# Optimization experiments

Hardware: AMD Instinct MI355X
Metric: run time of the kernel (lower is better)

Reference implementation:

```python
import jax, jax.numpy as jnp
import numpy as np

B, N, C = 8, 1374, 768
H = 12
HD = C // H  # 64
HIDDEN = int(C * 4.0)  # 3072
EPS = 1e-5


def setup_inputs() -> dict:
    key = jax.random.key(0)
    ks = jax.random.split(key, 12)
    s = 0.02
    return {
        "x": jax.random.normal(ks[0], (B, N, C), jnp.float32),
        "rope_freqs": jax.random.normal(ks[1], (1, N, 1, HD), jnp.float32),
        "ln1_g": jnp.ones((C,), jnp.float32),
        "ln1_b": jnp.zeros((C,), jnp.float32),
        "qkv_w": jax.random.normal(ks[2], (3 * C, C), jnp.float32) * s,
        "qkv_b": jnp.zeros((3 * C,), jnp.float32),
        "proj_w": jax.random.normal(ks[3], (C, C), jnp.float32) * s,
        "proj_b": jnp.zeros((C,), jnp.float32),
        "ln2_g": jnp.ones((C,), jnp.float32),
        "ln2_b": jnp.zeros((C,), jnp.float32),
        "w1": jax.random.normal(ks[4], (HIDDEN, C), jnp.float32) * s,
        "b1": jnp.zeros((HIDDEN,), jnp.float32),
        "w2": jax.random.normal(ks[5], (HIDDEN, C), jnp.float32) * s,
        "b2": jnp.zeros((HIDDEN,), jnp.float32),
        "w3": jax.random.normal(ks[6], (C, HIDDEN), jnp.float32) * s,
        "b3": jnp.zeros((C,), jnp.float32),
    }


def _layernorm(x, g, b):
    mu = jnp.mean(x, axis=-1, keepdims=True)
    var = jnp.mean(jnp.square(x - mu), axis=-1, keepdims=True)
    return (x - mu) * jax.lax.rsqrt(var + EPS) * g + b


def _rotate_half(x):
    x1, x2 = jnp.split(x, 2, axis=-1)
    return jnp.concatenate([-x2, x1], axis=-1)


def _apply_rope(q, k, freqs):
    # freqs: [1, N, 1, HD] -> [1, 1, N, HD] (matches torch permute(0,2,1,3))
    f = jnp.transpose(freqs, (0, 2, 1, 3))
    cos, sin = jnp.cos(f), jnp.sin(f)
    q_rot = q * cos + _rotate_half(q) * sin
    k_rot = k * cos + _rotate_half(k) * sin
    return q_rot, k_rot


def reference(x, rope_freqs, ln1_g, ln1_b, qkv_w, qkv_b, proj_w, proj_b,
              ln2_g, ln2_b, w1, b1, w2, b2, w3, b3):
    scale = HD ** -0.5
    # --- Attention branch ---
    h = _layernorm(x, ln1_g, ln1_b)
    qkv = jnp.einsum('bnc,dc->bnd', h, qkv_w) + qkv_b          # [B,N,3C]
    qkv = qkv.reshape(B, N, 3, H, HD).transpose(2, 0, 3, 1, 4)  # [3,B,H,N,HD]
    q, k, v = qkv[0], qkv[1], qkv[2]
    # rope_freqs covers all N tokens -> n_special = 0 path
    q, k = _apply_rope(q, k, rope_freqs)
    attn = jnp.einsum('bhnd,bhmd->bhnm', q, k) * scale          # [B,H,N,N]
    attn = jax.nn.softmax(attn, axis=-1)
    o = jnp.einsum('bhnm,bhmd->bhnd', attn, v)                  # [B,H,N,HD]
    o = o.transpose(0, 2, 1, 3).reshape(B, N, C)
    o = jnp.einsum('bnc,dc->bnd', o, proj_w) + proj_b
    x = x + o
    # --- SwiGLU MLP branch ---
    h2 = _layernorm(x, ln2_g, ln2_b)
    x1 = jnp.einsum('bnc,hc->bnh', h2, w1) + b1
    x2 = jnp.einsum('bnc,hc->bnh', h2, w2) + b2
    hid = jax.nn.silu(x1) * x2
    mlp_out = jnp.einsum('bnh,ch->bnc', hid, w3) + b3
    return x + mlp_out
```

## Files before the change

### kernel.cpp

```cpp
#include <hip/hip_runtime.h>
#include <stdint.h>

#define B_ 8
#define N_ 1374
#define C_ 768
#define H_ 12
#define HD_ 64
#define HID_ 3072
#define M_ (B_*N_)
#define MPAD_ 11008
#define QT_ 22
#define QT2_ 11

typedef __attribute__((ext_vector_type(8))) short short8;
typedef __attribute__((ext_vector_type(4))) float f32x4;
typedef __attribute__((ext_vector_type(4))) _Float16 half4;

__device__ __forceinline__ unsigned short f2bf(float f) {
  unsigned u = __float_as_uint(f);
  u += 0x7FFF + ((u >> 16) & 1);
  return (unsigned short)(u >> 16);
}
__device__ __forceinline__ float bf2f(unsigned short h) {
  return __uint_as_float(((unsigned)h) << 16);
}

#if __has_builtin(__builtin_amdgcn_global_load_lds)
#define HAVE_GLL 1
#endif

__device__ __forceinline__ void gld16(const unsigned short* g, unsigned short* l) {
#ifdef HAVE_GLL
  __builtin_amdgcn_global_load_lds((const __attribute__((address_space(1))) void*)g,
                                   (__attribute__((address_space(3))) void*)l, 16, 0, 0);
#else
  *(short8*)l = *(const short8*)g;
#endif
}

__global__ __launch_bounds__(256) void cvt_kernel(const float* __restrict__ in,
                                                  unsigned short* __restrict__ out, int n4) {
  int id = blockIdx.x * 256 + threadIdx.x;
  if (id >= n4) return;
  float4 v = ((const float4*)in)[id];
  ushort4 o;
  o.x = f2bf(v.x); o.y = f2bf(v.y); o.z = f2bf(v.z); o.w = f2bf(v.w);
  ((ushort4*)out)[id] = o;
}

__global__ __launch_bounds__(256) void ln_kernel(const float* __restrict__ in,
    const float* __restrict__ g, const float* __restrict__ bta,
    unsigned short* __restrict__ out) {
  int row = blockIdx.x;
  int t = threadIdx.x;
  const float* xr = in + (size_t)row * C_;
  float v0 = xr[t], v1 = xr[t + 256], v2 = xr[t + 512];
  float s1 = v0 + v1 + v2;
  float s2 = v0*v0 + v1*v1 + v2*v2;
  for (int off = 1; off < 64; off <<= 1) {
    s1 += __shfl_xor(s1, off, 64);
    s2 += __shfl_xor(s2, off, 64);
  }
  __shared__ float r1[4], r2[4];
  int wave = t >> 6, lane = t & 63;
  if (lane == 0) { r1[wave] = s1; r2[wave] = s2; }
  __syncthreads();
  float tot1 = r1[0] + r1[1] + r1[2] + r1[3];
  float tot2 = r2[0] + r2[1] + r2[2] + r2[3];
  float mu = tot1 * (1.0f / C_);
  float var = tot2 * (1.0f / C_) - mu * mu;
  float rs = rsqrtf(var + 1e-5f);
  size_t ob = (size_t)row * C_;
  out[ob + t]       = f2bf((v0 - mu) * rs * g[t]       + bta[t]);
  out[ob + t + 256] = f2bf((v1 - mu) * rs * g[t + 256] + bta[t + 256]);
  out[ob + t + 512] = f2bf((v2 - mu) * rs * g[t + 512] + bta[t + 512]);
}

template<int EPI>
__global__ __launch_bounds__(256, 2) void gemm_bt(
    const unsigned short* __restrict__ A,
    const unsigned short* __restrict__ W,
    void* __restrict__ outp,
    const float* __restrict__ bias0,
    const float* __restrict__ resid,
    int K, int ldo, int Mvalid)
{
  __shared__ __align__(16) unsigned short As[4096];
  __shared__ __align__(16) unsigned short Bs[4096];
  const int t = threadIdx.x;
  const int lane = t & 63;
  const int wave = t >> 6;
  const int wm = (wave >> 1) * 64;
  const int wn = (wave & 1) * 64;
  const int lr = lane & 15;
  const int lk = (lane >> 4) * 8;
  const int tm0 = blockIdx.y * 128;
  const int tn0 = blockIdx.x * 128;
  const int r0 = t >> 2;
  const int c0 = (t & 3) * 8;
  const unsigned short* ga0 = A + (size_t)(tm0 + r0) * K + c0;
  const unsigned short* ga1 = A + (size_t)(tm0 + 64 + r0) * K + c0;
  const unsigned short* gb0 = W + (size_t)(tn0 + r0) * K + c0;
  const unsigned short* gb1 = W + (size_t)(tn0 + 64 + r0) * K + c0;
  f32x4 zero = {0.f, 0.f, 0.f, 0.f};
  f32x4 acc[4][4];
#pragma unroll
  for (int mi = 0; mi < 4; ++mi)
#pragma unroll
    for (int ni = 0; ni < 4; ++ni) acc[mi][ni] = zero;

  for (int kt = 0; kt < K; kt += 32) {
    __syncthreads();
    gld16(ga0 + kt, &As[t * 8]);
    gld16(ga1 + kt, &As[2048 + t * 8]);
    gld16(gb0 + kt, &Bs[t * 8]);
    gld16(gb1 + kt, &Bs[2048 + t * 8]);
    __syncthreads();
    short8 af[4], bfr[4];
#pragma unroll
    for (int mi = 0; mi < 4; ++mi) af[mi] = *(const short8*)&As[(wm + mi * 16 + lr) * 32 + lk];
#pragma unroll
    for (int ni = 0; ni < 4; ++ni) bfr[ni] = *(const short8*)&Bs[(wn + ni * 16 + lr) * 32 + lk];
#pragma unroll
    for (int mi = 0; mi < 4; ++mi)
#pragma unroll
      for (int ni = 0; ni < 4; ++ni)
        acc[mi][ni] = __builtin_amdgcn_mfma_f32_16x16x32_bf16(af[mi], bfr[ni], acc[mi][ni], 0, 0, 0);
  }
#pragma unroll
  for (int mi = 0; mi < 4; ++mi) {
#pragma unroll
    for (int ni = 0; ni < 4; ++ni) {
      int col = tn0 + wn + ni * 16 + lr;
      float bval = bias0[col];
#pragma unroll
      for (int r = 0; r < 4; ++r) {
        int row = tm0 + wm + mi * 16 + (lane >> 4) * 4 + r;
        float v = acc[mi][ni][r] + bval;
        size_t idx = (size_t)row * ldo + col;
        if (EPI == 0) {
          ((unsigned short*)outp)[idx] = f2bf(v);
        } else if (EPI == 1) {
          if (row < Mvalid) ((float*)outp)[idx] = resid[idx] + v;
        } else {
          if (row < Mvalid) ((float*)outp)[idx] = ((float*)outp)[idx] + v;
        }
      }
    }
  }
}

__global__ __launch_bounds__(256, 2) void gemm_w12_swiglu(
    const unsigned short* __restrict__ A,
    const unsigned short* __restrict__ W1,
    const unsigned short* __restrict__ W2,
    unsigned short* __restrict__ hid,
    const float* __restrict__ b1,
    const float* __restrict__ b2)
{
  __shared__ __align__(16) unsigned short As[4096];
  __shared__ __align__(16) unsigned short B1s[2048];
  __shared__ __align__(16) unsigned short B2s[2048];
  const int t = threadIdx.x;
  const int lane = t & 63;
  const int wave = t >> 6;
  const int wm = (wave >> 1) * 64;
  const int wn = (wave & 1) * 32;
  const int lr = lane & 15;
  const int lg = lane >> 4;
  const int lk = lg * 8;
  const int tm0 = blockIdx.y * 128;
  const int tn0 = blockIdx.x * 64;
  const int r0 = t >> 2;
  const int c0 = (t & 3) * 8;
  const unsigned short* ga0 = A + (size_t)(tm0 + r0) * 768 + c0;
  const unsigned short* ga1 = A + (size_t)(tm0 + 64 + r0) * 768 + c0;
  const unsigned short* g1 = W1 + (size_t)(tn0 + r0) * 768 + c0;
  const unsigned short* g2 = W2 + (size_t)(tn0 + r0) * 768 + c0;
  f32x4 zero = {0.f, 0.f, 0.f, 0.f};
  f32x4 acc1[4][2], acc2[4][2];
#pragma unroll
  for (int mi = 0; mi < 4; ++mi)
#pragma unroll
    for (int ni = 0; ni < 2; ++ni) { acc1[mi][ni] = zero; acc2[mi][ni] = zero; }

  for (int kt = 0; kt < 768; kt += 32) {
    __syncthreads();
    gld16(ga0 + kt, &As[t * 8]);
    gld16(ga1 + kt, &As[2048 + t * 8]);
    gld16(g1 + kt, &B1s[t * 8]);
    gld16(g2 + kt, &B2s[t * 8]);
    __syncthreads();
    short8 af[4], b1f[2], b2f[2];
#pragma unroll
    for (int mi = 0; mi < 4; ++mi) af[mi] = *(const short8*)&As[(wm + mi * 16 + lr) * 32 + lk];
#pragma unroll
    for (int ni = 0; ni < 2; ++ni) {
      b1f[ni] = *(const short8*)&B1s[(wn + ni * 16 + lr) * 32 + lk];
      b2f[ni] = *(const short8*)&B2s[(wn + ni * 16 + lr) * 32 + lk];
    }
#pragma unroll
    for (int mi = 0; mi < 4; ++mi)
#pragma unroll
      for (int ni = 0; ni < 2; ++ni) {
        acc1[mi][ni] = __builtin_amdgcn_mfma_f32_16x16x32_bf16(af[mi], b1f[ni], acc1[mi][ni], 0, 0, 0);
        acc2[mi][ni] = __builtin_amdgcn_mfma_f32_16x16x32_bf16(af[mi], b2f[ni], acc2[mi][ni], 0, 0, 0);
      }
  }
#pragma unroll
  for (int mi = 0; mi < 4; ++mi) {
#pragma unroll
    for (int ni = 0; ni < 2; ++ni) {
      int col = tn0 + wn + ni * 16 + lr;
      float bv1 = b1[col], bv2 = b2[col];
#pragma unroll
      for (int r = 0; r < 4; ++r) {
        int row = tm0 + wm + mi * 16 + lg * 4 + r;
        float a1 = acc1[mi][ni][r] + bv1;
        float a2 = acc2[mi][ni][r] + bv2;
        float h = a1 / (1.f + __expf(-a1)) * a2;
        hid[(size_t)row * HID_ + col] = f2bf(h);
      }
    }
  }
}

__global__ __launch_bounds__(256) void rope_kernel(unsigned short* __restrict__ qkv,
                                                   const float* __restrict__ freqs) {
  int id = blockIdx.x * 256 + threadIdx.x;
  int e = id & 31;
  int hm = id >> 5;
  int head = hm % H_;
  int m = hm / H_;
  int n = m % N_;
  float f1 = freqs[n * HD_ + e];
  float f2 = freqs[n * HD_ + e + 32];
  float c1 = cosf(f1), s1 = sinf(f1);
  float c2 = cosf(f2), s2 = sinf(f2);
  unsigned short* base = qkv + (size_t)m * 2304 + head * HD_ + e;
#pragma unroll
  for (int part = 0; part < 2; ++part) {
    unsigned short* p = base + part * 768;
    float x1 = bf2f(p[0]);
    float x2 = bf2f(p[32]);
    p[0]  = f2bf(x1 * c1 - x2 * s1);
    p[32] = f2bf(x2 * c2 + x1 * s2);
  }
}

__global__ __launch_bounds__(256, 2) void attn_kernel(
    const unsigned short* __restrict__ qkv,
    unsigned short* __restrict__ o2)
{
  __shared__ __align__(16) unsigned short Ks[64 * 80];
  __shared__ __align__(16) _Float16 Vt[64 * 72];
  int bidx = blockIdx.x;
  int qt = bidx % QT2_;
  int bh = bidx / QT2_;
  int head = bh % H_;
  int b = bh / H_;
  int t = threadIdx.x, lane = t & 63, wave = t >> 6;
  int lr = lane & 15, lg = lane >> 4;

  short8 bq[2][2];
#pragma unroll
  for (int s = 0; s < 2; ++s) {
    int m = qt * 128 + wave * 32 + s * 16 + lr;
    int mc = (m < N_) ? m : (N_ - 1);
    const unsigned short* qrow = qkv + (size_t)(b * N_ + mc) * 2304 + head * HD_;
    bq[s][0] = *(const short8*)(qrow + lg * 8);
    bq[s][1] = *(const short8*)(qrow + 32 + lg * 8);
  }

  f32x4 zero = {0.f, 0.f, 0.f, 0.f};
  f32x4 acc[2][4];
#pragma unroll
  for (int s = 0; s < 2; ++s)
#pragma unroll
    for (int dt = 0; dt < 4; ++dt) acc[s][dt] = zero;
  float den[2] = {0.f, 0.f};

  const int vp = t & 31;
  const int vc = t >> 5;

  for (int jt = 0; jt < QT_; ++jt) {
    __syncthreads();
#pragma unroll
    for (int u = t; u < 512; u += 256) {
      int row = u >> 3, c = u & 7;
      int j = jt * 64 + row;
      int jc = (j < N_) ? j : (N_ - 1);
      const unsigned short* src = qkv + (size_t)(b * N_ + jc) * 2304 + 768 + head * HD_ + c * 8;
      *(short8*)&Ks[row * 80 + c * 8] = *(const short8*)src;
    }
    {
      int j0 = jt * 64 + 2 * vp;
      int j1 = j0 + 1;
      int j0c = (j0 < N_) ? j0 : (N_ - 1);
      int j1c = (j1 < N_) ? j1 : (N_ - 1);
      const unsigned short* s0 = qkv + (size_t)(b * N_ + j0c) * 2304 + 1536 + head * HD_ + vc * 8;
      const unsigned short* s1 = qkv + (size_t)(b * N_ + j1c) * 2304 + 1536 + head * HD_ + vc * 8;
      short8 v0 = *(const short8*)s0;
      short8 v1 = *(const short8*)s1;
#pragma unroll
      for (int i = 0; i < 8; ++i) {
        _Float16 lo = (_Float16)bf2f((unsigned short)v0[i]);
        _Float16 hi = (_Float16)bf2f((unsigned short)v1[i]);
        unsigned w = (unsigned)__builtin_bit_cast(unsigned short, lo)
                   | ((unsigned)__builtin_bit_cast(unsigned short, hi) << 16);
        *(unsigned*)&Vt[(vc * 8 + i) * 72 + 2 * vp] = w;
      }
    }
    __syncthreads();
#pragma unroll
    for (int st = 0; st < 4; ++st) {
      short8 ak0 = *(const short8*)&Ks[(st * 16 + lr) * 80 + lg * 8];
      short8 ak1 = *(const short8*)&Ks[(st * 16 + lr) * 80 + 32 + lg * 8];
      int jb = jt * 64 + st * 16 + lg * 4;
      half4 pf[2];
#pragma unroll
      for (int s = 0; s < 2; ++s) {
        f32x4 sc = zero;
        sc = __builtin_amdgcn_mfma_f32_16x16x32_bf16(ak0, bq[s][0], sc, 0, 0, 0);
        sc = __builtin_amdgcn_mfma_f32_16x16x32_bf16(ak1, bq[s][1], sc, 0, 0, 0);
        float dsum = 0.f;
#pragma unroll
        for (int r = 0; r < 4; ++r) {
          float pv = (jb + r < N_) ? __expf(sc[r] * 0.125f) : 0.f;
          dsum += pv;
          pf[s][r] = (_Float16)pv;
        }
        den[s] += dsum;
      }
#pragma unroll
      for (int dt = 0; dt < 4; ++dt) {
        half4 bv = *(const half4*)&Vt[(dt * 16 + lr) * 72 + st * 16 + lg * 4];
        acc[0][dt] = __builtin_amdgcn_mfma_f32_16x16x16f16(pf[0], bv, acc[0][dt], 0, 0, 0);
        acc[1][dt] = __builtin_amdgcn_mfma_f32_16x16x16f16(pf[1], bv, acc[1][dt], 0, 0, 0);
      }
    }
  }
#pragma unroll
  for (int s = 0; s < 2; ++s) {
    den[s] += __shfl_xor(den[s], 16, 64);
    den[s] += __shfl_xor(den[s], 32, 64);
  }
#pragma unroll
  for (int s = 0; s < 2; ++s) {
#pragma unroll
    for (int r = 0; r < 4; ++r) {
      float dm = __shfl(den[s], lg * 4 + r, 64);
      int m = qt * 128 + wave * 32 + s * 16 + lg * 4 + r;
      if (m < N_) {
        float invd = 1.f / dm;
        unsigned short* orow = o2 + (size_t)(b * N_ + m) * C_ + head * HD_;
#pragma unroll
        for (int dt = 0; dt < 4; ++dt)
          orow[dt * 16 + lr] = f2bf(acc[s][dt][r] * invd);
      }
    }
  }
}

extern "C" void kernel_launch(void* const* d_in, const int* in_sizes, int n_in,
                              void* d_out, int out_size, void* d_ws, size_t ws_size,
                              hipStream_t stream) {
  const float* x      = (const float*)d_in[0];
  const float* freqs  = (const float*)d_in[1];
  const float* ln1_g  = (const float*)d_in[2];
  const float* ln1_b  = (const float*)d_in[3];
  const float* qkv_w  = (const float*)d_in[4];
  const float* qkv_b  = (const float*)d_in[5];
  const float* proj_w = (const float*)d_in[6];
  const float* proj_b = (const float*)d_in[7];
  const float* ln2_g  = (const float*)d_in[8];
  const float* ln2_b  = (const float*)d_in[9];
  const float* w1     = (const float*)d_in[10];
  const float* b1     = (const float*)d_in[11];
  const float* w2     = (const float*)d_in[12];
  const float* b2     = (const float*)d_in[13];
  const float* w3     = (const float*)d_in[14];
  const float* b3     = (const float*)d_in[15];
  float* out = (float*)d_out;
  char* ws = (char*)d_ws;

  unsigned short* hB     = (unsigned short*)(ws + 0);
  unsigned short* wqkvB  = (unsigned short*)(ws + 16908288);
  unsigned short* wprojB = (unsigned short*)(ws + 20447232);
  unsigned short* w12B   = (unsigned short*)(ws + 21626880);
  unsigned short* w3B    = (unsigned short*)(ws + 31064064);
  unsigned short* qkvB   = (unsigned short*)(ws + 35782656);
  unsigned short* o2B    = (unsigned short*)(ws + 86507520);
  unsigned short* hidB   = qkvB;

  cvt_kernel<<<1728, 256, 0, stream>>>(qkv_w, wqkvB, 2304 * 768 / 4);
  cvt_kernel<<<576,  256, 0, stream>>>(proj_w, wprojB, 768 * 768 / 4);
  cvt_kernel<<<2304, 256, 0, stream>>>(w1, w12B, 3072 * 768 / 4);
  cvt_kernel<<<2304, 256, 0, stream>>>(w2, w12B + 3072 * 768, 3072 * 768 / 4);
  cvt_kernel<<<2304, 256, 0, stream>>>(w3, w3B, 768 * 3072 / 4);

  ln_kernel<<<M_, 256, 0, stream>>>(x, ln1_g, ln1_b, hB);
  gemm_bt<0><<<dim3(18, 86), 256, 0, stream>>>(hB, wqkvB, qkvB, qkv_b, nullptr, 768, 2304, M_);
  rope_kernel<<<16488, 256, 0, stream>>>(qkvB, freqs);
  attn_kernel<<<B_ * H_ * QT2_, 256, 0, stream>>>(qkvB, o2B);
  gemm_bt<1><<<dim3(6, 86), 256, 0, stream>>>(o2B, wprojB, out, proj_b, x, 768, 768, M_);

  ln_kernel<<<M_, 256, 0, stream>>>(out, ln2_g, ln2_b, hB);
  gemm_w12_swiglu<<<dim3(48, 86), 256, 0, stream>>>(hB, w12B, w12B + 3072 * 768, hidB, b1, b2);
  gemm_bt<3><<<dim3(6, 86), 256, 0, stream>>>(hidB, w3B, out, b3, nullptr, 3072, 768, M_);
}
```

Baseline: 627.5 us.

## Fuse RoPE into QKV GEMM epilogue, merge weight casts, widen GEMM K-step

Removes the standalone rope kernel by applying rotary embedding in the QKV GEMM epilogue, pairing accumulator columns d and d+32 within each wave's 64-column head slice. The five weight-conversion launches become one kernel that dispatches on index range. Both GEMM main loops now load two 32-wide K slices per barrier pair, halving the synchronisation count at the cost of doubled LDS per block, which may reduce occupancy. The fused epilogue uses fast __sincosf and recomputes sin/cos per output element, which adds some transcendental work and precision risk.

Measured after the change: 598.7 us. -4.6%, faster.

```diff
diff --git a/kernel.cpp b/kernel.cpp
--- a/kernel.cpp
+++ b/kernel.cpp
@@ -38,11 +38,18 @@
 #endif
 }
 
-__global__ __launch_bounds__(256) void cvt_kernel(const float* __restrict__ in,
-                                                  unsigned short* __restrict__ out, int n4) {
+__global__ __launch_bounds__(256) void cvt5_kernel(
+    const float* __restrict__ s0, const float* __restrict__ s1,
+    const float* __restrict__ s2, const float* __restrict__ s3,
+    const float* __restrict__ s4, unsigned short* __restrict__ out) {
   int id = blockIdx.x * 256 + threadIdx.x;
-  if (id >= n4) return;
-  float4 v = ((const float4*)in)[id];
+  const float* src; int off;
+  if (id < 442368)        { src = s0; off = id; }
+  else if (id < 589824)   { src = s1; off = id - 442368; }
+  else if (id < 1179648)  { src = s2; off = id - 589824; }
+  else if (id < 1769472)  { src = s3; off = id - 1179648; }
+  else                    { src = s4; off = id - 1769472; }
+  float4 v = ((const float4*)src)[off];
   ushort4 o;
   o.x = f2bf(v.x); o.y = f2bf(v.y); o.z = f2bf(v.z); o.w = f2bf(v.w);
   ((ushort4*)out)[id] = o;
@@ -76,24 +83,26 @@
   out[ob + t + 512] = f2bf((v2 - mu) * rs * g[t + 512] + bta[t + 512]);
 }
 
-template<int EPI>
+template<int EPI, int ROPE>
 __global__ __launch_bounds__(256, 2) void gemm_bt(
     const unsigned short* __restrict__ A,
     const unsigned short* __restrict__ W,
     void* __restrict__ outp,
     const float* __restrict__ bias0,
     const float* __restrict__ resid,
+    const float* __restrict__ freqs,
     int K, int ldo, int Mvalid)
 {
-  __shared__ __align__(16) unsigned short As[4096];
-  __shared__ __align__(16) unsigned short Bs[4096];
+  __shared__ __align__(16) unsigned short As[2][4096];
+  __shared__ __align__(16) unsigned short Bs[2][4096];
   const int t = threadIdx.x;
   const int lane = t & 63;
   const int wave = t >> 6;
   const int wm = (wave >> 1) * 64;
   const int wn = (wave & 1) * 64;
   const int lr = lane & 15;
-  const int lk = (lane >> 4) * 8;
+  const int lg = lane >> 4;
+  const int lk = lg * 8;
   const int tm0 = blockIdx.y * 128;
   const int tn0 = blockIdx.x * 128;
   const int r0 = t >> 2;
@@ -109,41 +118,81 @@
 #pragma unroll
     for (int ni = 0; ni < 4; ++ni) acc[mi][ni] = zero;
 
-  for (int kt = 0; kt < K; kt += 32) {
-    __syncthreads();
-    gld16(ga0 + kt, &As[t * 8]);
-    gld16(ga1 + kt, &As[2048 + t * 8]);
-    gld16(gb0 + kt, &Bs[t * 8]);
-    gld16(gb1 + kt, &Bs[2048 + t * 8]);
-    __syncthreads();
-    short8 af[4], bfr[4];
-#pragma unroll
-    for (int mi = 0; mi < 4; ++mi) af[mi] = *(const short8*)&As[(wm + mi * 16 + lr) * 32 + lk];
-#pragma unroll
-    for (int ni = 0; ni < 4; ++ni) bfr[ni] = *(const short8*)&Bs[(wn + ni * 16 + lr) * 32 + lk];
-#pragma unroll
-    for (int mi = 0; mi < 4; ++mi)
-#pragma unroll
-      for (int ni = 0; ni < 4; ++ni)
-        acc[mi][ni] = __builtin_amdgcn_mfma_f32_16x16x32_bf16(af[mi], bfr[ni], acc[mi][ni], 0, 0, 0);
-  }
-#pragma unroll
-  for (int mi = 0; mi < 4; ++mi) {
-#pragma unroll
-    for (int ni = 0; ni < 4; ++ni) {
-      int col = tn0 + wn + ni * 16 + lr;
-      float bval = bias0[col];
-#pragma unroll
-      for (int r = 0; r < 4; ++r) {
-        int row = tm0 + wm + mi * 16 + (lane >> 4) * 4 + r;
-        float v = acc[mi][ni][r] + bval;
-        size_t idx = (size_t)row * ldo + col;
-        if (EPI == 0) {
-          ((unsigned short*)outp)[idx] = f2bf(v);
-        } else if (EPI == 1) {
-          if (row < Mvalid) ((float*)outp)[idx] = resid[idx] + v;
-        } else {
-          if (row < Mvalid) ((float*)outp)[idx] = ((float*)outp)[idx] + v;
+  for (int kt = 0; kt < K; kt += 64) {
+    __syncthreads();
+    gld16(ga0 + kt,      &As[0][t * 8]);
+    gld16(ga1 + kt,      &As[0][2048 + t * 8]);
+    gld16(ga0 + kt + 32, &As[1][t * 8]);
+    gld16(ga1 + kt + 32, &As[1][2048 + t * 8]);
+    gld16(gb0 + kt,      &Bs[0][t * 8]);
+    gld16(gb1 + kt,      &Bs[0][2048 + t * 8]);
+    gld16(gb0 + kt + 32, &Bs[1][t * 8]);
+    gld16(gb1 + kt + 32, &Bs[1][2048 + t * 8]);
+    __syncthreads();
+#pragma unroll
+    for (int u = 0; u < 2; ++u) {
+      short8 af[4], bfr[4];
+#pragma unroll
+      for (int mi = 0; mi < 4; ++mi) af[mi] = *(const short8*)&As[u][(wm + mi * 16 + lr) * 32 + lk];
+#pragma unroll
+      for (int ni = 0; ni < 4; ++ni) bfr[ni] = *(const short8*)&Bs[u][(wn + ni * 16 + lr) * 32 + lk];
+#pragma unroll
+      for (int mi = 0; mi < 4; ++mi)
+#pragma unroll
+        for (int ni = 0; ni < 4; ++ni)
+          acc[mi][ni] = __builtin_amdgcn_mfma_f32_16x16x32_bf16(af[mi], bfr[ni], acc[mi][ni], 0, 0, 0);
+    }
+  }
+
+  if (EPI == 0) {
+    bool dorope = ROPE && ((tn0 + wn) < 1536);
+#pragma unroll
+    for (int mi = 0; mi < 4; ++mi) {
+#pragma unroll
+      for (int p = 0; p < 2; ++p) {
+        int col1 = tn0 + wn + p * 16 + lr;
+        int col2 = col1 + 32;
+        float bv1 = bias0[col1], bv2 = bias0[col2];
+        int e = p * 16 + lr;
+#pragma unroll
+        for (int r = 0; r < 4; ++r) {
+          int row = tm0 + wm + mi * 16 + lg * 4 + r;
+          float v1 = acc[mi][p][r] + bv1;
+          float v2 = acc[mi][p + 2][r] + bv2;
+          float o1 = v1, o2 = v2;
+          if (dorope) {
+            int n = row % N_;
+            float f1 = freqs[n * HD_ + e];
+            float f2 = freqs[n * HD_ + e + 32];
+            float c1, s1, c2, s2;
+            __sincosf(f1, &s1, &c1);
+            __sincosf(f2, &s2, &c2);
+            o1 = v1 * c1 - v2 * s1;
+            o2 = v2 * c2 + v1 * s2;
+          }
+          size_t base = (size_t)row * ldo;
+          ((unsigned short*)outp)[base + col1] = f2bf(o1);
+          ((unsigned short*)outp)[base + col2] = f2bf(o2);
+        }
+      }
+    }
+  } else {
+#pragma unroll
+    for (int mi = 0; mi < 4; ++mi) {
+#pragma unroll
+      for (int ni = 0; ni < 4; ++ni) {
+        int col = tn0 + wn + ni * 16 + lr;
+        float bval = bias0[col];
+#pragma unroll
+        for (int r = 0; r < 4; ++r) {
+          int row = tm0 + wm + mi * 16 + lg * 4 + r;
+          float v = acc[mi][ni][r] + bval;
+          size_t idx = (size_t)row * ldo + col;
+          if (EPI == 1) {
+            if (row < Mvalid) ((float*)outp)[idx] = resid[idx] + v;
+          } else {
+            if (row < Mvalid) ((float*)outp)[idx] = ((float*)outp)[idx] + v;
+          }
         }
       }
     }
@@ -158,9 +207,9 @@
     const float* __restrict__ b1,
     const float* __restrict__ b2)
 {
-  __shared__ __align__(16) unsigned short As[4096];
-  __shared__ __align__(16) unsigned short B1s[2048];
-  __shared__ __align__(16) unsigned short B2s[2048];
+  __shared__ __align__(16) unsigned short As[2][4096];
+  __shared__ __align__(16) unsigned short B1s[2][2048];
+  __shared__ __align__(16) unsigned short B2s[2][2048];
   const int t = threadIdx.x;
   const int lane = t & 63;
   const int wave = t >> 6;
@@ -184,28 +233,35 @@
 #pragma unroll
     for (int ni = 0; ni < 2; ++ni) { acc1[mi][ni] = zero; acc2[mi][ni] = zero; }
 
-  for (int kt = 0; kt < 768; kt += 32) {
-    __syncthreads();
-    gld16(ga0 + kt, &As[t * 8]);
-    gld16(ga1 + kt, &As[2048 + t * 8]);
-    gld16(g1 + kt, &B1s[t * 8]);
-    gld16(g2 + kt, &B2s[t * 8]);
-    __syncthreads();
-    short8 af[4], b1f[2], b2f[2];
-#pragma unroll
-    for (int mi = 0; mi < 4; ++mi) af[mi] = *(const short8*)&As[(wm + mi * 16 + lr) * 32 + lk];
-#pragma unroll
-    for (int ni = 0; ni < 2; ++ni) {
-      b1f[ni] = *(const short8*)&B1s[(wn + ni * 16 + lr) * 32 + lk];
-      b2f[ni] = *(const short8*)&B2s[(wn + ni * 16 + lr) * 32 + lk];
-    }
-#pragma unroll
-    for (int mi = 0; mi < 4; ++mi)
+  for (int kt = 0; kt < 768; kt += 64) {
+    __syncthreads();
+    gld16(ga0 + kt,      &As[0][t * 8]);
+    gld16(ga1 + kt,      &As[0][2048 + t * 8]);
+    gld16(ga0 + kt + 32, &As[1][t * 8]);
+    gld16(ga1 + kt + 32, &As[1][2048 + t * 8]);
+    gld16(g1 + kt,       &B1s[0][t * 8]);
+    gld16(g1 + kt + 32,  &B1s[1][t * 8]);
+    gld16(g2 + kt,       &B2s[0][t * 8]);
+    gld16(g2 + kt + 32,  &B2s[1][t * 8]);
+    __syncthreads();
+#pragma unroll
+    for (int u = 0; u < 2; ++u) {
+      short8 af[4], b1f[2], b2f[2];
+#pragma unroll
+      for (int mi = 0; mi < 4; ++mi) af[mi] = *(const short8*)&As[u][(wm + mi * 16 + lr) * 32 + lk];
 #pragma unroll
       for (int ni = 0; ni < 2; ++ni) {
-        acc1[mi][ni] = __builtin_amdgcn_mfma_f32_16x16x32_bf16(af[mi], b1f[ni], acc1[mi][ni], 0, 0, 0);
-        acc2[mi][ni] = __builtin_amdgcn_mfma_f32_16x16x32_bf16(af[mi], b2f[ni], acc2[mi][ni], 0, 0, 0);
-      }
+        b1f[ni] = *(const short8*)&B1s[u][(wn + ni * 16 + lr) * 32 + lk];
+        b2f[ni] = *(const short8*)&B2s[u][(wn + ni * 16 + lr) * 32 + lk];
+      }
+#pragma unroll
+      for (int mi = 0; mi < 4; ++mi)
+#pragma unroll
+        for (int ni = 0; ni < 2; ++ni) {
+          acc1[mi][ni] = __builtin_amdgcn_mfma_f32_16x16x32_bf16(af[mi], b1f[ni], acc1[mi][ni], 0, 0, 0);
+          acc2[mi][ni] = __builtin_amdgcn_mfma_f32_16x16x32_bf16(af[mi], b2f[ni], acc2[mi][ni], 0, 0, 0);
+        }
+    }
   }
 #pragma unroll
   for (int mi = 0; mi < 4; ++mi) {
@@ -222,29 +278,6 @@
         hid[(size_t)row * HID_ + col] = f2bf(h);
       }
     }
-  }
-}
-
-__global__ __launch_bounds__(256) void rope_kernel(unsigned short* __restrict__ qkv,
-                                                   const float* __restrict__ freqs) {
-  int id = blockIdx.x * 256 + threadIdx.x;
-  int e = id & 31;
-  int hm = id >> 5;
-  int head = hm % H_;
-  int m = hm / H_;
-  int n = m % N_;
-  float f1 = freqs[n * HD_ + e];
-  float f2 = freqs[n * HD_ + e + 32];
-  float c1 = cosf(f1), s1 = sinf(f1);
-  float c2 = cosf(f2), s2 = sinf(f2);
-  unsigned short* base = qkv + (size_t)m * 2304 + head * HD_ + e;
-#pragma unroll
-  for (int part = 0; part < 2; ++part) {
-    unsigned short* p = base + part * 768;
-    float x1 = bf2f(p[0]);
-    float x2 = bf2f(p[32]);
-    p[0]  = f2bf(x1 * c1 - x2 * s1);
-    p[32] = f2bf(x2 * c2 + x1 * s2);
   }
 }
 
@@ -393,19 +426,14 @@
   unsigned short* o2B    = (unsigned short*)(ws + 86507520);
   unsigned short* hidB   = qkvB;
 
-  cvt_kernel<<<1728, 256, 0, stream>>>(qkv_w, wqkvB, 2304 * 768 / 4);
-  cvt_kernel<<<576,  256, 0, stream>>>(proj_w, wprojB, 768 * 768 / 4);
-  cvt_kernel<<<2304, 256, 0, stream>>>(w1, w12B, 3072 * 768 / 4);
-  cvt_kernel<<<2304, 256, 0, stream>>>(w2, w12B + 3072 * 768, 3072 * 768 / 4);
-  cvt_kernel<<<2304, 256, 0, stream>>>(w3, w3B, 768 * 3072 / 4);
+  cvt5_kernel<<<9216, 256, 0, stream>>>(qkv_w, proj_w, w1, w2, w3, wqkvB);
 
   ln_kernel<<<M_, 256, 0, stream>>>(x, ln1_g, ln1_b, hB);
-  gemm_bt<0><<<dim3(18, 86), 256, 0, stream>>>(hB, wqkvB, qkvB, qkv_b, nullptr, 768, 2304, M_);
-  rope_kernel<<<16488, 256, 0, stream>>>(qkvB, freqs);
+  gemm_bt<0, 1><<<dim3(18, 86), 256, 0, stream>>>(hB, wqkvB, qkvB, qkv_b, nullptr, freqs, 768, 2304, M_);
   attn_kernel<<<B_ * H_ * QT2_, 256, 0, stream>>>(qkvB, o2B);
-  gemm_bt<1><<<dim3(6, 86), 256, 0, stream>>>(o2B, wprojB, out, proj_b, x, 768, 768, M_);
+  gemm_bt<1, 0><<<dim3(6, 86), 256, 0, stream>>>(o2B, wprojB, out, proj_b, x, nullptr, 768, 768, M_);
 
   ln_kernel<<<M_, 256, 0, stream>>>(out, ln2_g, ln2_b, hB);
   gemm_w12_swiglu<<<dim3(48, 86), 256, 0, stream>>>(hB, w12B, w12B + 3072 * 768, hidB, b1, b2);
-  gemm_bt<3><<<dim3(6, 86), 256, 0, stream>>>(hidB, w3B, out, b3, nullptr, 3072, 768, M_);
-}
+  gemm_bt<3, 0><<<dim3(6, 86), 256, 0, stream>>>(hidB, w3B, out, b3, nullptr, nullptr, 3072, 768, M_);
+}
```
